# Kernel tuning notes

Hardware: AMD Instinct MI355X
Metric: run time of the kernel (lower is better)

Reference implementation:

```python
import jax, jax.numpy as jnp
import numpy as np

B, N, D = 4096, 64, 128


def setup_inputs() -> dict:
    key = jax.random.key(0)
    ks = jax.random.split(key, 7)
    return {
        "query_emb": jax.random.normal(ks[0], (B, D), jnp.float32),
        "refer_embs": jax.random.normal(ks[1], (B, N, D), jnp.float32),
        "query_r": jax.random.normal(ks[2], (B, D), jnp.float32),
        "refer_r": jax.random.normal(ks[3], (B, N, D), jnp.float32),
        "start_embs": jax.random.normal(ks[4], (B, N, D), jnp.float32),
        "W1": jax.random.normal(ks[5], (D, 2 * D), jnp.float32) * (6.0 / (3 * D)) ** 0.5,  # xavier-ish
        "b1": jnp.zeros((D,), jnp.float32),
        "W2": jax.random.normal(ks[6], (D, D), jnp.float32) * (6.0 / (2 * D)) ** 0.5,
        "b2": jnp.zeros((D,), jnp.float32),
    }


def reference(query_emb, refer_embs, query_r, refer_r, start_embs, W1, b1, W2, b2):
    # bias term per neighbor: [B, N, D]
    bias = refer_embs - start_embs * refer_r
    # broadcast query relation to neighbors and concat -> [B, N, 2D]
    qr = jnp.broadcast_to(query_r[:, None, :], refer_r.shape)
    cat = jnp.concatenate([qr, refer_r], axis=-1)
    h1 = jax.nn.relu(jnp.einsum('bnk,dk->bnd', cat, W1) + b1)
    attn = jnp.einsum('bnk,dk->bnd', h1, W2) + b2
    # weighted sum over neighbor dim -> [B, D]
    final_refer = jnp.sum(attn * bias, axis=-2)
    ref_norm = jnp.sum(jnp.abs(final_refer), axis=-1, keepdims=True)
    query_norm = jnp.sum(jnp.abs(query_emb), axis=-1, keepdims=True)
    const = 2.5
    final_refer = final_refer / (1e-9 + ref_norm / query_norm * const)
    return query_emb + final_refer
```

## Files before the change

### kernel.cpp

```cpp
#include <hip/hip_runtime.h>
#include <hip/hip_bf16.h>


typedef __attribute__((ext_vector_type(8))) short bf16x8;
typedef __attribute__((ext_vector_type(4))) float f32x4;

#define WG_BARRIER()                                            \
    do {                                                        \
        asm volatile("s_waitcnt lgkmcnt(0)" ::: "memory");      \
        __builtin_amdgcn_s_barrier();                           \
    } while (0)

__device__ __forceinline__ unsigned short f2bf(float x) {
    unsigned int u = __float_as_uint(x);
    u += 0x7FFFu + ((u >> 16) & 1u);
    return (unsigned short)(u >> 16);
}
__device__ __forceinline__ unsigned int pack2bf(float lo, float hi) {
    unsigned int ulo = __float_as_uint(lo) + 0x8000u;
    unsigned int uhi = __float_as_uint(hi) + 0x8000u;
    return (ulo >> 16) | (uhi & 0xFFFF0000u);
}

__global__ __launch_bounds__(256) void pa_prep(const float* __restrict__ W1,
                                               const float* __restrict__ W2,
                                               unsigned short* __restrict__ w1b,
                                               unsigned short* __restrict__ w2b) {
    int i = blockIdx.x * 256 + threadIdx.x;
    if (i < 16384) {
        int d = i >> 7, k = i & 127;
        w1b[i] = f2bf(W1[d * 256 + 128 + k]);
    } else {
        int j = i - 16384;
        w2b[j] = f2bf(W2[j]);
    }
}

__global__ __launch_bounds__(256) void pa_qv(const float* __restrict__ query_r,
                                             const float* __restrict__ W1,
                                             const float* __restrict__ b1,
                                             float* __restrict__ qv) {
    __shared__ float wa[128][129];
    __shared__ float sq[32][128];
    const int tid = threadIdx.x;
    const int b0 = blockIdx.x * 32;

    for (int i = tid; i < 128 * 128; i += 256) {
        int d = i >> 7, k = i & 127;
        wa[d][k] = W1[d * 256 + k];
    }
    for (int i = tid; i < 32 * 128; i += 256) {
        sq[i >> 7][i & 127] = query_r[(size_t)b0 * 128 + i];
    }
    __syncthreads();

    const int d = tid & 127;
    const int rb = (tid >> 7) * 16;
    const float bb = b1[d];
    for (int j = 0; j < 16; ++j) {
        int r = rb + j;
        float a0 = 0.f, a1 = 0.f, a2 = 0.f, a3 = 0.f;
        #pragma unroll
        for (int k = 0; k < 128; k += 4) {
            a0 += sq[r][k + 0] * wa[d][k + 0];
            a1 += sq[r][k + 1] * wa[d][k + 1];
            a2 += sq[r][k + 2] * wa[d][k + 2];
            a3 += sq[r][k + 3] * wa[d][k + 3];
        }
        qv[(size_t)(b0 + r) * 128 + d] = bb + ((a0 + a1) + (a2 + a3));
    }
}

__global__ __launch_bounds__(256, 2) void pa_main(
    const float* __restrict__ query_emb,
    const float* __restrict__ refer_embs,
    const float* __restrict__ refer_r,
    const float* __restrict__ start_embs,
    const float* __restrict__ qv,
    const unsigned short* __restrict__ w1b,
    const unsigned short* __restrict__ w2b,
    const float* __restrict__ b2,
    float* __restrict__ out) {
    __shared__ __align__(16) float sR[64 * 128];
    __shared__ __align__(16) unsigned short sH[64 * 128];
    __shared__ float sFin[128];
    __shared__ float sRed[4];

    const int b    = blockIdx.x;
    const int tid  = threadIdx.x;
    const int lane = tid & 63;
    const int wv   = tid >> 6;
    const int hl   = lane & 15;
    const int qh   = lane >> 4;
    const int wcol = wv * 32;

    const size_t base = (size_t)b * 8192;

    float qe   = (tid < 128) ? query_emb[(size_t)b * 128 + tid] : 0.f;
    float qv0  = qv[(size_t)b * 128 + wcol + hl];
    float qv1  = qv[(size_t)b * 128 + wcol + 16 + hl];
    float b2v0 = b2[wcol + hl];
    float b2v1 = b2[wcol + 16 + hl];
    bf16x8 bW[2][4], bW2[2][4];
    #pragma unroll
    for (int ct = 0; ct < 2; ++ct)
        #pragma unroll
        for (int ks = 0; ks < 4; ++ks) {
            bW [ct][ks] = *(const bf16x8*)(w1b + (wcol + ct * 16 + hl) * 128 + ks * 32 + qh * 8);
            bW2[ct][ks] = *(const bf16x8*)(w2b + (wcol + ct * 16 + hl) * 128 + ks * 32 + qh * 8);
        }

    {
        const float* gR = refer_r + base;
        #pragma unroll
        for (int i = 0; i < 8; ++i) {
            int row   = wv * 16 + 2 * i + (lane >> 5);
            int chunk = (lane & 31) ^ (row & 7);
            __builtin_amdgcn_global_load_lds(
                (const __attribute__((address_space(1))) unsigned int*)(gR + row * 128 + chunk * 4),
                (__attribute__((address_space(3))) unsigned int*)(sR + wv * 2048 + i * 256),
                16, 0, 0);
        }
    }
    __syncthreads();

    float fe[32], fs[32];
    {
        const float* gE = refer_embs + base;
        const float* gS = start_embs + base;
        #pragma unroll
        for (int ct = 0; ct < 2; ++ct)
            #pragma unroll
            for (int rt = 0; rt < 4; ++rt)
                #pragma unroll
                for (int j = 0; j < 4; ++j) {
                    int row = rt * 16 + qh * 4 + j;
                    int col = wcol + ct * 16 + hl;
                    int o   = row * 128 + col;
                    fe[ct * 16 + rt * 4 + j] = gE[o];
                    fs[ct * 16 + rt * 4 + j] = gS[o];
                }
    }

    f32x4 acc1[4][2] = {};
    #pragma unroll
    for (int rt = 0; rt < 4; ++rt) {
        const int row = rt * 16 + hl;
        const int sw  = row & 7;
        const float* rowp = sR + row * 128;
        bf16x8 af[4];
        #pragma unroll
        for (int ks = 0; ks < 4; ++ks) {
            int c0 = ks * 8 + qh * 2;
            float4 fa = *(const float4*)(rowp + ((c0    ) ^ sw) * 4);
            float4 fb = *(const float4*)(rowp + ((c0 + 1) ^ sw) * 4);
            union { unsigned int u[4]; bf16x8 v; } cv;
            cv.u[0] = pack2bf(fa.x, fa.y);
            cv.u[1] = pack2bf(fa.z, fa.w);
            cv.u[2] = pack2bf(fb.x, fb.y);
            cv.u[3] = pack2bf(fb.z, fb.w);
            af[ks] = cv.v;
        }
        #pragma unroll
        for (int ct = 0; ct < 2; ++ct)
            #pragma unroll
            for (int ks = 0; ks < 4; ++ks)
                acc1[rt][ct] = __builtin_amdgcn_mfma_f32_16x16x32_bf16(af[ks], bW[ct][ks], acc1[rt][ct], 0, 0, 0);
    }

    #pragma unroll
    for (int ct = 0; ct < 2; ++ct) {
        const int col = wcol + ct * 16 + hl;
        const float q = (ct == 0) ? qv0 : qv1;
        #pragma unroll
        for (int rt = 0; rt < 4; ++rt) {
            #pragma unroll
            for (int j = 0; j < 4; ++j) {
                int row = rt * 16 + qh * 4 + j;
                float h = acc1[rt][ct][j] + q;
                h = h > 0.0f ? h : 0.0f;
                int byte = row * 256 + ((col * 2) ^ ((row & 7) << 4));
                *(unsigned short*)((char*)sH + byte) = f2bf(h);
            }
        }
    }
    WG_BARRIER();

    f32x4 acc2[4][2] = {};
    #pragma unroll
    for (int rt = 0; rt < 4; ++rt) {
        const int row = rt * 16 + hl;
        const int rsw = (row & 7) << 4;
        bf16x8 af[4];
        #pragma unroll
        for (int ks = 0; ks < 4; ++ks) {
            int byte = row * 256 + ((ks * 64 + qh * 16) ^ rsw);
            af[ks] = *(const bf16x8*)((const char*)sH + byte);
        }
        #pragma unroll
        for (int ct = 0; ct < 2; ++ct)
            #pragma unroll
            for (int ks = 0; ks < 4; ++ks)
                acc2[rt][ct] = __builtin_amdgcn_mfma_f32_16x16x32_bf16(af[ks], bW2[ct][ks], acc2[rt][ct], 0, 0, 0);
    }

    float p0 = 0.f, p1 = 0.f;
    #pragma unroll
    for (int ct = 0; ct < 2; ++ct) {
        const int col = wcol + ct * 16 + hl;
        const float bb = (ct == 0) ? b2v0 : b2v1;
        const int cch = col >> 2, cdw = col & 3;
        float pp = 0.f;
        #pragma unroll
        for (int rt = 0; rt < 4; ++rt) {
            #pragma unroll
            for (int j = 0; j < 4; ++j) {
                int row  = rt * 16 + qh * 4 + j;
                float rv = sR[row * 128 + ((cch ^ (row & 7)) << 2) + cdw];
                float e  = fe[ct * 16 + rt * 4 + j];
                float s  = fs[ct * 16 + rt * 4 + j];
                pp += (acc2[rt][ct][j] + bb) * (e - s * rv);
            }
        }
        if (ct == 0) p0 = pp; else p1 = pp;
    }
    p0 += __shfl_xor(p0, 16); p0 += __shfl_xor(p0, 32);
    p1 += __shfl_xor(p1, 16); p1 += __shfl_xor(p1, 32);
    if (qh == 0) {
        sFin[wcol + hl]      = p0;
        sFin[wcol + 16 + hl] = p1;
    }
    WG_BARRIER();

    float fv = 0.f;
    if (tid < 128) {
        fv = sFin[tid];
        float rn = fabsf(fv), qn = fabsf(qe);
        #pragma unroll
        for (int off = 1; off < 64; off <<= 1) {
            rn += __shfl_xor(rn, off);
            qn += __shfl_xor(qn, off);
        }
        if (lane == 0) { sRed[wv * 2] = rn; sRed[wv * 2 + 1] = qn; }
    }
    WG_BARRIER();
    if (tid < 128) {
        float RN = sRed[0] + sRed[2];
        float QN = sRed[1] + sRed[3];
        float scale = 1.0f / (1e-9f + (RN / QN) * 2.5f);
        out[(size_t)b * 128 + tid] = qe + fv * scale;
    }
}

extern "C" void kernel_launch(void* const* d_in, const int* in_sizes, int n_in,
                              void* d_out, int out_size, void* d_ws, size_t ws_size,
                              hipStream_t stream) {
    const float* query_emb  = (const float*)d_in[0];
    const float* refer_embs = (const float*)d_in[1];
    const float* query_r    = (const float*)d_in[2];
    const float* refer_r    = (const float*)d_in[3];
    const float* start_embs = (const float*)d_in[4];
    const float* W1         = (const float*)d_in[5];
    const float* b1         = (const float*)d_in[6];
    const float* W2         = (const float*)d_in[7];
    const float* b2         = (const float*)d_in[8];
    float* out = (float*)d_out;

    char* ws = (char*)d_ws;
    float* qv            = (float*)ws;
    unsigned short* w1b  = (unsigned short*)(ws + 2 * 1024 * 1024);
    unsigned short* w2b  = w1b + 16384;

    pa_prep<<<128, 256, 0, stream>>>(W1, W2, w1b, w2b);
    pa_qv<<<128, 256, 0, stream>>>(query_r, W1, b1, qv);
    pa_main<<<4096, 256, 0, stream>>>(query_emb, refer_embs, refer_r, start_embs,
                                      qv, w1b, w2b, b2, out);
}
```

Before: 115.9 us.

## Split work by row tiles per wave instead of column slices, shrink LDS

Each wave now owns 16 neighbor rows across all 128 output columns instead of all 64 rows across 32 columns. refer_r is loaded straight to registers rather than staged in LDS, and the hidden tile lives in per-wave LDS, so no block barrier is needed between the two GEMMs. Per-wave partial sums are combined through shared memory at the end. Weights are now read from global/L2 inside the loops rather than preloaded, refer_r is read twice, and occupancy is raised to three blocks per SM, which risks more L2 traffic and register pressure.

```diff
diff --git a/kernel.cpp b/kernel.cpp
--- a/kernel.cpp
+++ b/kernel.cpp
@@ -4,12 +4,6 @@
 
 typedef __attribute__((ext_vector_type(8))) short bf16x8;
 typedef __attribute__((ext_vector_type(4))) float f32x4;
-
-#define WG_BARRIER()                                            \
-    do {                                                        \
-        asm volatile("s_waitcnt lgkmcnt(0)" ::: "memory");      \
-        __builtin_amdgcn_s_barrier();                           \
-    } while (0)
 
 __device__ __forceinline__ unsigned short f2bf(float x) {
     unsigned int u = __float_as_uint(x);
@@ -71,7 +65,7 @@
     }
 }
 
-__global__ __launch_bounds__(256, 2) void pa_main(
+__global__ __launch_bounds__(256, 3) void pa_main(
     const float* __restrict__ query_emb,
     const float* __restrict__ refer_embs,
     const float* __restrict__ refer_r,
@@ -81,9 +75,8 @@
     const unsigned short* __restrict__ w2b,
     const float* __restrict__ b2,
     float* __restrict__ out) {
-    __shared__ __align__(16) float sR[64 * 128];
-    __shared__ __align__(16) unsigned short sH[64 * 128];
-    __shared__ float sFin[128];
+    __shared__ __align__(16) unsigned short sT[4][16 * 128];
+    __shared__ float sFin[4][128];
     __shared__ float sRed[4];
 
     const int b    = blockIdx.x;
@@ -92,149 +85,136 @@
     const int wv   = tid >> 6;
     const int hl   = lane & 15;
     const int qh   = lane >> 4;
-    const int wcol = wv * 32;
 
     const size_t base = (size_t)b * 8192;
 
-    float qe   = (tid < 128) ? query_emb[(size_t)b * 128 + tid] : 0.f;
-    float qv0  = qv[(size_t)b * 128 + wcol + hl];
-    float qv1  = qv[(size_t)b * 128 + wcol + 16 + hl];
-    float b2v0 = b2[wcol + hl];
-    float b2v1 = b2[wcol + 16 + hl];
-    bf16x8 bW[2][4], bW2[2][4];
-    #pragma unroll
-    for (int ct = 0; ct < 2; ++ct)
+    float qe = (tid < 128) ? query_emb[(size_t)b * 128 + tid] : 0.f;
+    float qvr[8], b2r[8];
+    #pragma unroll
+    for (int ct = 0; ct < 8; ++ct) {
+        qvr[ct] = qv[(size_t)b * 128 + ct * 16 + hl];
+        b2r[ct] = b2[ct * 16 + hl];
+    }
+
+    bf16x8 af[4];
+    {
+        const float* gR = refer_r + base + (size_t)(wv * 16 + hl) * 128;
+        float4 ra[8];
         #pragma unroll
         for (int ks = 0; ks < 4; ++ks) {
-            bW [ct][ks] = *(const bf16x8*)(w1b + (wcol + ct * 16 + hl) * 128 + ks * 32 + qh * 8);
-            bW2[ct][ks] = *(const bf16x8*)(w2b + (wcol + ct * 16 + hl) * 128 + ks * 32 + qh * 8);
-        }
+            ra[ks * 2]     = *(const float4*)(gR + ks * 32 + qh * 8);
+            ra[ks * 2 + 1] = *(const float4*)(gR + ks * 32 + qh * 8 + 4);
+        }
+        #pragma unroll
+        for (int ks = 0; ks < 4; ++ks) {
+            union { unsigned int u[4]; bf16x8 v; } cv;
+            cv.u[0] = pack2bf(ra[ks * 2].x,     ra[ks * 2].y);
+            cv.u[1] = pack2bf(ra[ks * 2].z,     ra[ks * 2].w);
+            cv.u[2] = pack2bf(ra[ks * 2 + 1].x, ra[ks * 2 + 1].y);
+            cv.u[3] = pack2bf(ra[ks * 2 + 1].z, ra[ks * 2 + 1].w);
+            af[ks] = cv.v;
+        }
+    }
+
+    f32x4 acc1[8] = {};
+    #pragma unroll
+    for (int ct = 0; ct < 8; ++ct) {
+        const unsigned short* wp = w1b + (size_t)(ct * 16 + hl) * 128 + qh * 8;
+        bf16x8 w0 = *(const bf16x8*)(wp);
+        bf16x8 w1 = *(const bf16x8*)(wp + 32);
+        bf16x8 w2 = *(const bf16x8*)(wp + 64);
+        bf16x8 w3 = *(const bf16x8*)(wp + 96);
+        acc1[ct] = __builtin_amdgcn_mfma_f32_16x16x32_bf16(af[0], w0, acc1[ct], 0, 0, 0);
+        acc1[ct] = __builtin_amdgcn_mfma_f32_16x16x32_bf16(af[1], w1, acc1[ct], 0, 0, 0);
+        acc1[ct] = __builtin_amdgcn_mfma_f32_16x16x32_bf16(af[2], w2, acc1[ct], 0, 0, 0);
+        acc1[ct] = __builtin_amdgcn_mfma_f32_16x16x32_bf16(af[3], w3, acc1[ct], 0, 0, 0);
+    }
 
     {
-        const float* gR = refer_r + base;
-        #pragma unroll
-        for (int i = 0; i < 8; ++i) {
-            int row   = wv * 16 + 2 * i + (lane >> 5);
-            int chunk = (lane & 31) ^ (row & 7);
-            __builtin_amdgcn_global_load_lds(
-                (const __attribute__((address_space(1))) unsigned int*)(gR + row * 128 + chunk * 4),
-                (__attribute__((address_space(3))) unsigned int*)(sR + wv * 2048 + i * 256),
-                16, 0, 0);
-        }
-    }
-    __syncthreads();
-
-    float fe[32], fs[32];
-    {
-        const float* gE = refer_embs + base;
-        const float* gS = start_embs + base;
-        #pragma unroll
-        for (int ct = 0; ct < 2; ++ct)
-            #pragma unroll
-            for (int rt = 0; rt < 4; ++rt)
-                #pragma unroll
-                for (int j = 0; j < 4; ++j) {
-                    int row = rt * 16 + qh * 4 + j;
-                    int col = wcol + ct * 16 + hl;
-                    int o   = row * 128 + col;
-                    fe[ct * 16 + rt * 4 + j] = gE[o];
-                    fs[ct * 16 + rt * 4 + j] = gS[o];
-                }
-    }
-
-    f32x4 acc1[4][2] = {};
-    #pragma unroll
-    for (int rt = 0; rt < 4; ++rt) {
-        const int row = rt * 16 + hl;
-        const int sw  = row & 7;
-        const float* rowp = sR + row * 128;
-        bf16x8 af[4];
-        #pragma unroll
-        for (int ks = 0; ks < 4; ++ks) {
-            int c0 = ks * 8 + qh * 2;
-            float4 fa = *(const float4*)(rowp + ((c0    ) ^ sw) * 4);
-            float4 fb = *(const float4*)(rowp + ((c0 + 1) ^ sw) * 4);
-            union { unsigned int u[4]; bf16x8 v; } cv;
-            cv.u[0] = pack2bf(fa.x, fa.y);
-            cv.u[1] = pack2bf(fa.z, fa.w);
-            cv.u[2] = pack2bf(fb.x, fb.y);
-            cv.u[3] = pack2bf(fb.z, fb.w);
-            af[ks] = cv.v;
-        }
-        #pragma unroll
-        for (int ct = 0; ct < 2; ++ct)
-            #pragma unroll
-            for (int ks = 0; ks < 4; ++ks)
-                acc1[rt][ct] = __builtin_amdgcn_mfma_f32_16x16x32_bf16(af[ks], bW[ct][ks], acc1[rt][ct], 0, 0, 0);
-    }
-
-    #pragma unroll
-    for (int ct = 0; ct < 2; ++ct) {
-        const int col = wcol + ct * 16 + hl;
-        const float q = (ct == 0) ? qv0 : qv1;
-        #pragma unroll
-        for (int rt = 0; rt < 4; ++rt) {
+        unsigned short* sw = &sT[wv][0];
+        #pragma unroll
+        for (int ct = 0; ct < 8; ++ct) {
+            const int col = ct * 16 + hl;
             #pragma unroll
             for (int j = 0; j < 4; ++j) {
-                int row = rt * 16 + qh * 4 + j;
-                float h = acc1[rt][ct][j] + q;
+                int row = qh * 4 + j;
+                float h = acc1[ct][j] + qvr[ct];
                 h = h > 0.0f ? h : 0.0f;
                 int byte = row * 256 + ((col * 2) ^ ((row & 7) << 4));
-                *(unsigned short*)((char*)sH + byte) = f2bf(h);
+                *(unsigned short*)((char*)sw + byte) = f2bf(h);
             }
         }
     }
-    WG_BARRIER();
-
-    f32x4 acc2[4][2] = {};
-    #pragma unroll
-    for (int rt = 0; rt < 4; ++rt) {
-        const int row = rt * 16 + hl;
-        const int rsw = (row & 7) << 4;
-        bf16x8 af[4];
+
+    bf16x8 af2[4];
+    {
+        const unsigned short* sw = &sT[wv][0];
+        const int rsw = (hl & 7) << 4;
         #pragma unroll
         for (int ks = 0; ks < 4; ++ks) {
-            int byte = row * 256 + ((ks * 64 + qh * 16) ^ rsw);
-            af[ks] = *(const bf16x8*)((const char*)sH + byte);
-        }
-        #pragma unroll
-        for (int ct = 0; ct < 2; ++ct)
-            #pragma unroll
-            for (int ks = 0; ks < 4; ++ks)
-                acc2[rt][ct] = __builtin_amdgcn_mfma_f32_16x16x32_bf16(af[ks], bW2[ct][ks], acc2[rt][ct], 0, 0, 0);
-    }
-
-    float p0 = 0.f, p1 = 0.f;
-    #pragma unroll
-    for (int ct = 0; ct < 2; ++ct) {
-        const int col = wcol + ct * 16 + hl;
-        const float bb = (ct == 0) ? b2v0 : b2v1;
-        const int cch = col >> 2, cdw = col & 3;
-        float pp = 0.f;
-        #pragma unroll
-        for (int rt = 0; rt < 4; ++rt) {
+            int byte = hl * 256 + ((ks * 64 + qh * 16) ^ rsw);
+            af2[ks] = *(const bf16x8*)((const char*)sw + byte);
+        }
+    }
+
+    f32x4 acc2[8] = {};
+    #pragma unroll
+    for (int ct = 0; ct < 8; ++ct) {
+        const unsigned short* wp = w2b + (size_t)(ct * 16 + hl) * 128 + qh * 8;
+        bf16x8 w0 = *(const bf16x8*)(wp);
+        bf16x8 w1 = *(const bf16x8*)(wp + 32);
+        bf16x8 w2 = *(const bf16x8*)(wp + 64);
+        bf16x8 w3 = *(const bf16x8*)(wp + 96);
+        acc2[ct] = __builtin_amdgcn_mfma_f32_16x16x32_bf16(af2[0], w0, acc2[ct], 0, 0, 0);
+        acc2[ct] = __builtin_amdgcn_mfma_f32_16x16x32_bf16(af2[1], w1, acc2[ct], 0, 0, 0);
+        acc2[ct] = __builtin_amdgcn_mfma_f32_16x16x32_bf16(af2[2], w2, acc2[ct], 0, 0, 0);
+        acc2[ct] = __builtin_amdgcn_mfma_f32_16x16x32_bf16(af2[3], w3, acc2[ct], 0, 0, 0);
+    }
+
+    float p[8];
+    const float* gE = refer_embs + base;
+    const float* gS = start_embs + base;
+    const float* gR = refer_r + base;
+    #pragma unroll
+    for (int hf = 0; hf < 2; ++hf) {
+        float fe[16], fs[16], fr[16];
+        #pragma unroll
+        for (int c = 0; c < 4; ++c) {
+            const int col = (hf * 4 + c) * 16 + hl;
             #pragma unroll
             for (int j = 0; j < 4; ++j) {
-                int row  = rt * 16 + qh * 4 + j;
-                float rv = sR[row * 128 + ((cch ^ (row & 7)) << 2) + cdw];
-                float e  = fe[ct * 16 + rt * 4 + j];
-                float s  = fs[ct * 16 + rt * 4 + j];
-                pp += (acc2[rt][ct][j] + bb) * (e - s * rv);
+                int off = (wv * 16 + qh * 4 + j) * 128 + col;
+                fe[c * 4 + j] = gE[off];
+                fs[c * 4 + j] = gS[off];
+                fr[c * 4 + j] = gR[off];
             }
         }
-        if (ct == 0) p0 = pp; else p1 = pp;
-    }
-    p0 += __shfl_xor(p0, 16); p0 += __shfl_xor(p0, 32);
-    p1 += __shfl_xor(p1, 16); p1 += __shfl_xor(p1, 32);
+        #pragma unroll
+        for (int c = 0; c < 4; ++c) {
+            const int ct = hf * 4 + c;
+            float pp = 0.f;
+            #pragma unroll
+            for (int j = 0; j < 4; ++j) {
+                float bias = fe[c * 4 + j] - fs[c * 4 + j] * fr[c * 4 + j];
+                pp += (acc2[ct][j] + b2r[ct]) * bias;
+            }
+            p[ct] = pp;
+        }
+    }
+    #pragma unroll
+    for (int ct = 0; ct < 8; ++ct) {
+        p[ct] += __shfl_xor(p[ct], 16);
+        p[ct] += __shfl_xor(p[ct], 32);
+    }
     if (qh == 0) {
-        sFin[wcol + hl]      = p0;
-        sFin[wcol + 16 + hl] = p1;
-    }
-    WG_BARRIER();
+        #pragma unroll
+        for (int ct = 0; ct < 8; ++ct) sFin[wv][ct * 16 + hl] = p[ct];
+    }
+    __syncthreads();
 
     float fv = 0.f;
     if (tid < 128) {
-        fv = sFin[tid];
+        fv = sFin[0][tid] + sFin[1][tid] + sFin[2][tid] + sFin[3][tid];
         float rn = fabsf(fv), qn = fabsf(qe);
         #pragma unroll
         for (int off = 1; off < 64; off <<= 1) {
@@ -243,7 +223,7 @@
         }
         if (lane == 0) { sRed[wv * 2] = rn; sRed[wv * 2 + 1] = qn; }
     }
-    WG_BARRIER();
+    __syncthreads();
     if (tid < 128) {
         float RN = sRed[0] + sRed[2];
         float QN = sRed[1] + sRed[3];
```

Result: slower. 191.1 us (+64.8%).

## Make main kernel persistent with double-buffered async LDS staging of inputs

Applied to the files above, without the earlier changes.

Replaces the one-block-per-batch launch with 256 blocks of 512 threads. Each block loops over 16 batches in 32-row half-tiles. refer_r, refer_embs and start_embs are all streamed into LDS with global_load_lds into a double buffer, so the next tile's loads overlap compute on the current one. Each wave now owns a 16-column slice, and query vectors are staged once per block. The aim is to hide global memory latency on this bandwidth-bound kernel, at the cost of one block per CU, large LDS use, and several workgroup barriers per tile.

```diff
diff --git a/kernel.cpp b/kernel.cpp
--- a/kernel.cpp
+++ b/kernel.cpp
@@ -11,10 +11,19 @@
         __builtin_amdgcn_s_barrier();                           \
     } while (0)
 
+#define VWAIT(n)                                                        \
+    do {                                                                \
+        asm volatile("s_waitcnt vmcnt(" #n ")" ::: "memory");           \
+        __builtin_amdgcn_sched_barrier(0);                              \
+    } while (0)
+
 __device__ __forceinline__ unsigned short f2bf(float x) {
     unsigned int u = __float_as_uint(x);
     u += 0x7FFFu + ((u >> 16) & 1u);
     return (unsigned short)(u >> 16);
+}
+__device__ __forceinline__ float bf2f(unsigned short h) {
+    return __uint_as_float(((unsigned int)h) << 16);
 }
 __device__ __forceinline__ unsigned int pack2bf(float lo, float hi) {
     unsigned int ulo = __float_as_uint(lo) + 0x8000u;
@@ -71,7 +80,7 @@
     }
 }
 
-__global__ __launch_bounds__(256, 2) void pa_main(
+__global__ __launch_bounds__(512, 1) void pa_main(
     const float* __restrict__ query_emb,
     const float* __restrict__ refer_embs,
     const float* __restrict__ refer_r,
@@ -81,175 +90,177 @@
     const unsigned short* __restrict__ w2b,
     const float* __restrict__ b2,
     float* __restrict__ out) {
-    __shared__ __align__(16) float sR[64 * 128];
-    __shared__ __align__(16) unsigned short sH[64 * 128];
+    __shared__ __align__(16) float bufR[2][32 * 128];
+    __shared__ __align__(16) float bufE[2][32 * 128];
+    __shared__ __align__(16) float bufS[2][32 * 128];
+    __shared__ __align__(16) unsigned short sH[32 * 128];
+    __shared__ float sQv[16 * 128];
+    __shared__ float sQe[16 * 128];
     __shared__ float sFin[128];
     __shared__ float sRed[4];
 
-    const int b    = blockIdx.x;
+    const int bid  = blockIdx.x;
     const int tid  = threadIdx.x;
     const int lane = tid & 63;
     const int wv   = tid >> 6;
     const int hl   = lane & 15;
     const int qh   = lane >> 4;
-    const int wcol = wv * 32;
-
-    const size_t base = (size_t)b * 8192;
-
-    float qe   = (tid < 128) ? query_emb[(size_t)b * 128 + tid] : 0.f;
-    float qv0  = qv[(size_t)b * 128 + wcol + hl];
-    float qv1  = qv[(size_t)b * 128 + wcol + 16 + hl];
-    float b2v0 = b2[wcol + hl];
-    float b2v1 = b2[wcol + 16 + hl];
-    bf16x8 bW[2][4], bW2[2][4];
+    const int col  = wv * 16 + hl;
+
+    const size_t base0 = (size_t)bid * 16 * 8192;
+
+    bf16x8 bW[4], bW2[4];
     #pragma unroll
-    for (int ct = 0; ct < 2; ++ct)
-        #pragma unroll
-        for (int ks = 0; ks < 4; ++ks) {
-            bW [ct][ks] = *(const bf16x8*)(w1b + (wcol + ct * 16 + hl) * 128 + ks * 32 + qh * 8);
-            bW2[ct][ks] = *(const bf16x8*)(w2b + (wcol + ct * 16 + hl) * 128 + ks * 32 + qh * 8);
-        }
-
+    for (int ks = 0; ks < 4; ++ks) {
+        bW[ks]  = *(const bf16x8*)(w1b + (size_t)col * 128 + ks * 32 + qh * 8);
+        bW2[ks] = *(const bf16x8*)(w2b + (size_t)col * 128 + ks * 32 + qh * 8);
+    }
+    const float b2r = b2[col];
     {
-        const float* gR = refer_r + base;
-        #pragma unroll
-        for (int i = 0; i < 8; ++i) {
-            int row   = wv * 16 + 2 * i + (lane >> 5);
-            int chunk = (lane & 31) ^ (row & 7);
-            __builtin_amdgcn_global_load_lds(
-                (const __attribute__((address_space(1))) unsigned int*)(gR + row * 128 + chunk * 4),
-                (__attribute__((address_space(3))) unsigned int*)(sR + wv * 2048 + i * 256),
-                16, 0, 0);
-        }
+        const float4* gqv = (const float4*)(qv + (size_t)bid * 16 * 128);
+        const float4* gqe = (const float4*)(query_emb + (size_t)bid * 16 * 128);
+        float4 v1 = gqv[tid];
+        float4 v2 = gqe[tid];
+        *(float4*)(sQv + tid * 4) = v1;
+        *(float4*)(sQe + tid * 4) = v2;
     }
     __syncthreads();
 
-    float fe[32], fs[32];
-    {
-        const float* gE = refer_embs + base;
-        const float* gS = start_embs + base;
-        #pragma unroll
-        for (int ct = 0; ct < 2; ++ct)
-            #pragma unroll
-            for (int rt = 0; rt < 4; ++rt)
+    #define ISSUE(bi, t)                                                                    \
+        do {                                                                                \
+            const int bb_   = (t) >> 1;                                                     \
+            const size_t gb = base0 + (size_t)bb_ * 8192 + ((t) & 1) * 4096;                \
+            _Pragma("unroll")                                                               \
+            for (int k = 0; k < 2; ++k) {                                                   \
+                int f = wv * 64 + lane + k * 512;                                           \
+                int row = f >> 5, c = f & 31;                                               \
+                int srcf = (row * 32 + (c ^ (row & 7))) * 4;                                \
+                int dst  = (wv * 64 + k * 512) * 4;                                         \
+                __builtin_amdgcn_global_load_lds(                                           \
+                    (const __attribute__((address_space(1))) unsigned int*)(refer_r + gb + srcf), \
+                    (__attribute__((address_space(3))) unsigned int*)(&bufR[bi][dst]), 16, 0, 0); \
+                __builtin_amdgcn_global_load_lds(                                           \
+                    (const __attribute__((address_space(1))) unsigned int*)(refer_embs + gb + srcf), \
+                    (__attribute__((address_space(3))) unsigned int*)(&bufE[bi][dst]), 16, 0, 0); \
+                __builtin_amdgcn_global_load_lds(                                           \
+                    (const __attribute__((address_space(1))) unsigned int*)(start_embs + gb + srcf), \
+                    (__attribute__((address_space(3))) unsigned int*)(&bufS[bi][dst]), 16, 0, 0); \
+            }                                                                               \
+        } while (0)
+
+    ISSUE(0, 0);
+
+    float pacc = 0.f;
+
+    #pragma unroll 1
+    for (int t = 0; t < 32; ++t) {
+        const int cur = t & 1;
+        const int bb  = t >> 1;
+
+        if (t < 31) ISSUE(cur ^ 1, t + 1);
+        if (t < 31) { VWAIT(6); } else { VWAIT(0); }
+        __builtin_amdgcn_s_barrier();
+
+        f32x4 acc1[2] = {};
+        #pragma unroll
+        for (int rt = 0; rt < 2; ++rt) {
+            const int row = rt * 16 + hl;
+            const int sw  = row & 7;
+            const float* rp = &bufR[cur][row * 128];
+            bf16x8 af[4];
+            #pragma unroll
+            for (int ks = 0; ks < 4; ++ks) {
+                int c0 = ks * 8 + qh * 2;
+                float4 fa = *(const float4*)(rp + ((c0    ) ^ sw) * 4);
+                float4 fb = *(const float4*)(rp + ((c0 + 1) ^ sw) * 4);
+                union { unsigned int u[4]; bf16x8 v; } cv;
+                cv.u[0] = pack2bf(fa.x, fa.y);
+                cv.u[1] = pack2bf(fa.z, fa.w);
+                cv.u[2] = pack2bf(fb.x, fb.y);
+                cv.u[3] = pack2bf(fb.z, fb.w);
+                af[ks] = cv.v;
+            }
+            #pragma unroll
+            for (int ks = 0; ks < 4; ++ks)
+                acc1[rt] = __builtin_amdgcn_mfma_f32_16x16x32_bf16(af[ks], bW[ks], acc1[rt], 0, 0, 0);
+        }
+
+        {
+            const float qvv = sQv[bb * 128 + col];
+            #pragma unroll
+            for (int rt = 0; rt < 2; ++rt) {
                 #pragma unroll
                 for (int j = 0; j < 4; ++j) {
                     int row = rt * 16 + qh * 4 + j;
-                    int col = wcol + ct * 16 + hl;
-                    int o   = row * 128 + col;
-                    fe[ct * 16 + rt * 4 + j] = gE[o];
-                    fs[ct * 16 + rt * 4 + j] = gS[o];
+                    float h = acc1[rt][j] + qvv;
+                    h = h > 0.0f ? h : 0.0f;
+                    int byte = row * 256 + ((col * 2) ^ ((row & 7) << 4));
+                    *(unsigned short*)((char*)sH + byte) = f2bf(h);
                 }
-    }
-
-    f32x4 acc1[4][2] = {};
-    #pragma unroll
-    for (int rt = 0; rt < 4; ++rt) {
-        const int row = rt * 16 + hl;
-        const int sw  = row & 7;
-        const float* rowp = sR + row * 128;
-        bf16x8 af[4];
-        #pragma unroll
-        for (int ks = 0; ks < 4; ++ks) {
-            int c0 = ks * 8 + qh * 2;
-            float4 fa = *(const float4*)(rowp + ((c0    ) ^ sw) * 4);
-            float4 fb = *(const float4*)(rowp + ((c0 + 1) ^ sw) * 4);
-            union { unsigned int u[4]; bf16x8 v; } cv;
-            cv.u[0] = pack2bf(fa.x, fa.y);
-            cv.u[1] = pack2bf(fa.z, fa.w);
-            cv.u[2] = pack2bf(fb.x, fb.y);
-            cv.u[3] = pack2bf(fb.z, fb.w);
-            af[ks] = cv.v;
-        }
-        #pragma unroll
-        for (int ct = 0; ct < 2; ++ct)
+            }
+        }
+        WG_BARRIER();
+
+        f32x4 acc2[2] = {};
+        #pragma unroll
+        for (int rt = 0; rt < 2; ++rt) {
+            const int row = rt * 16 + hl;
+            const int rsw = (row & 7) << 4;
+            bf16x8 af2[4];
+            #pragma unroll
+            for (int ks = 0; ks < 4; ++ks) {
+                int byte = row * 256 + ((ks * 64 + qh * 16) ^ rsw);
+                af2[ks] = *(const bf16x8*)((const char*)sH + byte);
+            }
             #pragma unroll
             for (int ks = 0; ks < 4; ++ks)
-                acc1[rt][ct] = __builtin_amdgcn_mfma_f32_16x16x32_bf16(af[ks], bW[ct][ks], acc1[rt][ct], 0, 0, 0);
-    }
-
-    #pragma unroll
-    for (int ct = 0; ct < 2; ++ct) {
-        const int col = wcol + ct * 16 + hl;
-        const float q = (ct == 0) ? qv0 : qv1;
-        #pragma unroll
-        for (int rt = 0; rt < 4; ++rt) {
+                acc2[rt] = __builtin_amdgcn_mfma_f32_16x16x32_bf16(af2[ks], bW2[ks], acc2[rt], 0, 0, 0);
+        }
+
+        #pragma unroll
+        for (int rt = 0; rt < 2; ++rt) {
             #pragma unroll
             for (int j = 0; j < 4; ++j) {
                 int row = rt * 16 + qh * 4 + j;
-                float h = acc1[rt][ct][j] + q;
-                h = h > 0.0f ? h : 0.0f;
-                int byte = row * 256 + ((col * 2) ^ ((row & 7) << 4));
-                *(unsigned short*)((char*)sH + byte) = f2bf(h);
-            }
-        }
-    }
-    WG_BARRIER();
-
-    f32x4 acc2[4][2] = {};
-    #pragma unroll
-    for (int rt = 0; rt < 4; ++rt) {
-        const int row = rt * 16 + hl;
-        const int rsw = (row & 7) << 4;
-        bf16x8 af[4];
-        #pragma unroll
-        for (int ks = 0; ks < 4; ++ks) {
-            int byte = row * 256 + ((ks * 64 + qh * 16) ^ rsw);
-            af[ks] = *(const bf16x8*)((const char*)sH + byte);
-        }
-        #pragma unroll
-        for (int ct = 0; ct < 2; ++ct)
-            #pragma unroll
-            for (int ks = 0; ks < 4; ++ks)
-                acc2[rt][ct] = __builtin_amdgcn_mfma_f32_16x16x32_bf16(af[ks], bW2[ct][ks], acc2[rt][ct], 0, 0, 0);
-    }
-
-    float p0 = 0.f, p1 = 0.f;
-    #pragma unroll
-    for (int ct = 0; ct < 2; ++ct) {
-        const int col = wcol + ct * 16 + hl;
-        const float bb = (ct == 0) ? b2v0 : b2v1;
-        const int cch = col >> 2, cdw = col & 3;
-        float pp = 0.f;
-        #pragma unroll
-        for (int rt = 0; rt < 4; ++rt) {
-            #pragma unroll
-            for (int j = 0; j < 4; ++j) {
-                int row  = rt * 16 + qh * 4 + j;
-                float rv = sR[row * 128 + ((cch ^ (row & 7)) << 2) + cdw];
-                float e  = fe[ct * 16 + rt * 4 + j];
-                float s  = fs[ct * 16 + rt * 4 + j];
-                pp += (acc2[rt][ct][j] + bb) * (e - s * rv);
-            }
-        }
-        if (ct == 0) p0 = pp; else p1 = pp;
-    }
-    p0 += __shfl_xor(p0, 16); p0 += __shfl_xor(p0, 32);
-    p1 += __shfl_xor(p1, 16); p1 += __shfl_xor(p1, 32);
-    if (qh == 0) {
-        sFin[wcol + hl]      = p0;
-        sFin[wcol + 16 + hl] = p1;
-    }
-    WG_BARRIER();
-
-    float fv = 0.f;
-    if (tid < 128) {
-        fv = sFin[tid];
-        float rn = fabsf(fv), qn = fabsf(qe);
-        #pragma unroll
-        for (int off = 1; off < 64; off <<= 1) {
-            rn += __shfl_xor(rn, off);
-            qn += __shfl_xor(qn, off);
-        }
-        if (lane == 0) { sRed[wv * 2] = rn; sRed[wv * 2 + 1] = qn; }
-    }
-    WG_BARRIER();
-    if (tid < 128) {
-        float RN = sRed[0] + sRed[2];
-        float QN = sRed[1] + sRed[3];
-        float scale = 1.0f / (1e-9f + (RN / QN) * 2.5f);
-        out[(size_t)b * 128 + tid] = qe + fv * scale;
-    }
+                int fi  = row * 128 + (((col >> 2) ^ (row & 7)) << 2) + (col & 3);
+                float e = bufE[cur][fi];
+                float s = bufS[cur][fi];
+                float r = bufR[cur][fi];
+                pacc += (acc2[rt][j] + b2r) * (e - s * r);
+            }
+        }
+
+        if (t & 1) {
+            float p = pacc;
+            p += __shfl_xor(p, 16);
+            p += __shfl_xor(p, 32);
+            if (qh == 0) sFin[col] = p;
+            WG_BARRIER();
+            float fv = 0.f, qe = 0.f;
+            if (tid < 128) {
+                fv = sFin[tid];
+                qe = sQe[bb * 128 + tid];
+                float rn = fabsf(fv), qn = fabsf(qe);
+                #pragma unroll
+                for (int off = 1; off < 64; off <<= 1) {
+                    rn += __shfl_xor(rn, off);
+                    qn += __shfl_xor(qn, off);
+                }
+                if (lane == 0) { sRed[wv * 2] = rn; sRed[wv * 2 + 1] = qn; }
+            }
+            WG_BARRIER();
+            if (tid < 128) {
+                float RN = sRed[0] + sRed[2];
+                float QN = sRed[1] + sRed[3];
+                float scale = 1.0f / (1e-9f + (RN / QN) * 2.5f);
+                out[((size_t)bid * 16 + bb) * 128 + tid] = qe + fv * scale;
+            }
+            pacc = 0.f;
+        }
+
+        WG_BARRIER();
+    }
+    #undef ISSUE
 }
 
 extern "C" void kernel_launch(void* const* d_in, const int* in_sizes, int n_in,
@@ -273,6 +284,6 @@
 
     pa_prep<<<128, 256, 0, stream>>>(W1, W2, w1b, w2b);
     pa_qv<<<128, 256, 0, stream>>>(query_r, W1, b1, qv);
-    pa_main<<<4096, 256, 0, stream>>>(query_emb, refer_embs, refer_r, start_embs,
-                                      qv, w1b, w2b, b2, out);
-}
+    pa_main<<<256, 512, 0, stream>>>(query_emb, refer_embs, refer_r, start_embs,
+                                     qv, w1b, w2b, b2, out);
+}
```

After: 135.6 us. 17.0% more time.
